# Optimization experiments

Measured on AMD Instinct MI355X. Metric: run time of the kernel, lower is better.

## Reference

```python
import jax, jax.numpy as jnp
import numpy as np
import math

L, B = 1024, 256
SEQ_DIM, KMER_DIM, HID = 16, 256, 64
N_LAYERS = 2
IN_DIM = SEQ_DIM + KMER_DIM + 21  # 293


def _normalize(v, eps=1e-12):
    return v / jnp.maximum(jnp.linalg.norm(v, axis=-1, keepdims=True), eps)


def _nerf_rot(a, b, c):
    # rotation matrix with columns [bc, n x bc, n] from last three backbone points
    bc = _normalize(c - b)
    n = _normalize(jnp.cross(b - a, bc))
    return jnp.stack([bc, jnp.cross(n, bc), n], axis=-1)  # (..., 3, 3)


def pnerf(c_tilde, nfrag):
    # c_tilde: (3L, B, 3) SRF coordinates; parallelized natural extension of reference frame
    Ltot, batch = c_tilde.shape[0], c_tilde.shape[1]
    k = Ltot // nfrag
    # contiguous fragments of length k, folded into the batch dim: (k, nfrag*B, 3)
    x = c_tilde.reshape(nfrag, k, batch, 3).transpose(1, 0, 2, 3).reshape(k, nfrag * batch, 3)
    init = jnp.array([[-math.sqrt(0.5), math.sqrt(1.5), 0.0],
                      [-math.sqrt(2.0), 0.0, 0.0],
                      [0.0, 0.0, 0.0]], dtype=c_tilde.dtype)
    F = nfrag * batch
    carry0 = (jnp.broadcast_to(init[0], (F, 3)),
              jnp.broadcast_to(init[1], (F, 3)),
              jnp.broadcast_to(init[2], (F, 3)))

    def extend(carry, ct):
        a, b, c = carry
        R = _nerf_rot(a, b, c)                      # (F, 3, 3)
        d = c + jnp.einsum('fij,fj->fi', R, ct)     # (F, 3)
        return (b, c, d), d

    _, frag = jax.lax.scan(extend, carry0, x)        # (k, F, 3)
    frag = frag.reshape(k, nfrag, batch, 3).transpose(1, 0, 2, 3)  # (nfrag, k, B, 3)

    # assemble fragments sequentially; init frame is identity/origin so frag 0 passes through
    carryA = (jnp.broadcast_to(init[0], (batch, 3)),
              jnp.broadcast_to(init[1], (batch, 3)),
              jnp.broadcast_to(init[2], (batch, 3)))

    def assemble(carry, fr):
        a, b, c = carry
        R = _nerf_rot(a, b, c)                      # (B, 3, 3)
        y = c + jnp.einsum('bij,kbj->kbi', R, fr)   # (k, B, 3)
        return (y[-3], y[-2], y[-1]), y

    _, ys = jax.lax.scan(assemble, carryA, frag)     # (nfrag, k, B, 3)
    return ys.reshape(nfrag * k, batch, 3)


def setup_inputs() -> dict:
    key = jax.random.key(0)
    ks = jax.random.split(key, 12)
    s = 0.05
    return {
        'seq': jax.random.randint(ks[0], (L, B), 0, 20, dtype=jnp.int64),
        'kmer': jax.random.randint(ks[1], (L, B), 0, 22 ** 3, dtype=jnp.int64),
        'pssm': jax.random.uniform(ks[2], (L, B, 21), dtype=jnp.float32),
        'length': jax.random.randint(ks[3], (L,), 1, L, dtype=jnp.int64),
        'seq_embed': jax.random.normal(ks[4], (20, SEQ_DIM), dtype=jnp.float32) * s,
        'kmer_embed': jax.random.normal(ks[5], (22 ** 3, KMER_DIM), dtype=jnp.float32) * s,
        'W0': jax.random.normal(ks[6], (IN_DIM, HID), dtype=jnp.float32) * s,
        'b0': jnp.zeros((HID,), dtype=jnp.float32),
        'We': jax.random.normal(ks[7], (HID, HID), dtype=jnp.float32) * s,
        'be': jnp.zeros((HID,), dtype=jnp.float32),
        'W1': jax.random.normal(ks[8], (HID, 9), dtype=jnp.float32) * s,
        'b1': jnp.zeros((9,), dtype=jnp.float32),
    }


def reference(seq, kmer, pssm, length, seq_embed, kmer_embed, W0, b0, We, be, W1, b1):
    s = seq_embed[seq]                                   # (L, B, 16)
    km = kmer_embed[kmer]                                # (L, B, 256)
    h = jnp.concatenate([s, km, pssm], axis=2)           # (L, B, 293)
    h = h @ W0 + b0                                      # (L, B, 64)
    # torch list-multiplication shares the SAME Linear across the n_layers blocks
    for _ in range(N_LAYERS):
        h = jax.nn.relu(h @ We + be)                     # dropout is identity at eval
    srf = h @ W1 + b1                                    # (L, B, 9)
    Ld, Bd = srf.shape[0], srf.shape[1]
    srf = srf.reshape(Ld, Bd, 3, 3).transpose(0, 2, 1, 3).reshape(3 * Ld, Bd, 3)
    return pnerf(srf, int(math.sqrt(Ld)))
```

## Files before the change

### kernel.cpp

```cpp
#include <hip/hip_runtime.h>
#include <math.h>

typedef short bf16x8 __attribute__((ext_vector_type(8)));
typedef float f32x4  __attribute__((ext_vector_type(4)));

__device__ __forceinline__ unsigned short f2bf(float x) {
    unsigned int u = __float_as_uint(x);
    return (unsigned short)((u + 0x7FFFu + ((u >> 16) & 1u)) >> 16);
}
__device__ __forceinline__ float bf2f(unsigned short h) {
    return __uint_as_float(((unsigned int)h) << 16);
}
__device__ __forceinline__ void split2(float x, unsigned short& h, unsigned short& l) {
    h = f2bf(x);
    l = f2bf(x - bf2f(h));
}
__device__ __forceinline__ void split2t(float x, unsigned short& h, unsigned short& l) {
    unsigned int u = __float_as_uint(x);
    h = (unsigned short)(u >> 16);
    float r = x - __uint_as_float(u & 0xFFFF0000u);
    l = f2bf(r);
}

__device__ __forceinline__ int hsw(int row, int col) {
    return (row << 6) + ((((col >> 3) ^ (row & 7)) << 3) | (col & 7));
}

__device__ __forceinline__ float inv_norm3(float x, float y, float z) {
    float d = fmaf(x, x, fmaf(y, y, z * z));
    return rsqrtf(fmaxf(d, 1e-24f));
}
__device__ __forceinline__ float3 f3sub(float3 a, float3 b) {
    return make_float3(a.x - b.x, a.y - b.y, a.z - b.z);
}
__device__ __forceinline__ float3 f3cross(float3 a, float3 b) {
    return make_float3(a.y * b.z - a.z * b.y,
                       a.z * b.x - a.x * b.z,
                       a.x * b.y - a.y * b.x);
}
__device__ __forceinline__ void nerf_frame(const float3& A, const float3& Bv,
                                           const float3& C, float3& bc,
                                           float3& n, float3& m3) {
    float3 w  = f3sub(C, Bv);
    float3 v  = f3sub(Bv, A);
    float3 cr = f3cross(v, w);
    float iw = inv_norm3(w.x, w.y, w.z);
    float ic = inv_norm3(cr.x, cr.y, cr.z);
    bc = make_float3(w.x * iw, w.y * iw, w.z * iw);
    n  = make_float3(cr.x * ic, cr.y * ic, cr.z * ic);
    m3 = f3cross(n, bc);
}
__device__ __forceinline__ float3 nerf_place(const float3& C, const float3& bc,
                                             const float3& m3, const float3& n,
                                             float tx, float ty, float tz) {
    return make_float3(
        fmaf(m3.x, ty, fmaf(bc.x, tx, fmaf(n.x, tz, C.x))),
        fmaf(m3.y, ty, fmaf(bc.y, tx, fmaf(n.y, tz, C.y))),
        fmaf(m3.z, ty, fmaf(bc.z, tx, fmaf(n.z, tz, C.z))));
}

struct KParams {
    const int* seq; const int* kmer; const float* pssm;
    const float* se; const float* emb;
    const float* W0; const float* b0; const float* We; const float* be;
    const float* W1; const float* b1;
    float* kmerT; float* seqT; float* srf_t; float* fragbuf;
    float4* frames; float* FPbuf; float* out;
    unsigned short *WeTH, *WeTL, *W0pTH, *W0pTL, *W1TH, *W1TL;
};

__global__ __launch_bounds__(256) void tables_kernel(KParams P) {
    const int tid = threadIdx.x;
    const int vb  = blockIdx.x;
    if (vb < 167) {
        const int lane = tid & 63;
        const int wv   = __builtin_amdgcn_readfirstlane(tid >> 6);
        const int q    = lane >> 4;
        const int c16  = lane & 15;
        const int r0   = vb * 64;
        const int n    = wv * 16 + c16;

        bf16x8 BH[8], BL[8];
        #pragma unroll
        for (int kt8 = 0; kt8 < 8; ++kt8)
            #pragma unroll
            for (int j = 0; j < 8; ++j) {
                float w = P.W0[(16 + kt8 * 32 + q * 8 + j) * 64 + n];
                unsigned short h, l; split2t(w, h, l);
                BH[kt8][j] = (short)h; BL[kt8][j] = (short)l;
            }
        f32x4 acc[4];
        #pragma unroll
        for (int t = 0; t < 4; ++t) acc[t] = (f32x4){0.f, 0.f, 0.f, 0.f};
        #pragma unroll
        for (int kt8 = 0; kt8 < 8; ++kt8) {
            #pragma unroll
            for (int t = 0; t < 4; ++t) {
                int rr = r0 + t * 16 + c16;
                if (rr > 10647) rr = 10647;
                const float* ap = P.emb + rr * 256 + kt8 * 32 + q * 8;
                float4 a0 = *(const float4*)ap;
                float4 a1 = *(const float4*)(ap + 4);
                bf16x8 ah, al;
                unsigned short h, l;
                split2t(a0.x, h, l); ah[0] = (short)h; al[0] = (short)l;
                split2t(a0.y, h, l); ah[1] = (short)h; al[1] = (short)l;
                split2t(a0.z, h, l); ah[2] = (short)h; al[2] = (short)l;
                split2t(a0.w, h, l); ah[3] = (short)h; al[3] = (short)l;
                split2t(a1.x, h, l); ah[4] = (short)h; al[4] = (short)l;
                split2t(a1.y, h, l); ah[5] = (short)h; al[5] = (short)l;
                split2t(a1.z, h, l); ah[6] = (short)h; al[6] = (short)l;
                split2t(a1.w, h, l); ah[7] = (short)h; al[7] = (short)l;
                acc[t] = __builtin_amdgcn_mfma_f32_16x16x32_bf16(ah, BH[kt8], acc[t], 0, 0, 0);
                acc[t] = __builtin_amdgcn_mfma_f32_16x16x32_bf16(al, BH[kt8], acc[t], 0, 0, 0);
                acc[t] = __builtin_amdgcn_mfma_f32_16x16x32_bf16(ah, BL[kt8], acc[t], 0, 0, 0);
            }
        }
        #pragma unroll
        for (int t = 0; t < 4; ++t)
            #pragma unroll
            for (int r = 0; r < 4; ++r) {
                int row = r0 + t * 16 + q * 4 + r;
                if (row < 10648) P.kmerT[row * 64 + n] = acc[t][r];
            }
    } else if (vb < 172) {
        int e = (vb - 167) * 256 + tid;
        int r = e >> 6, j = e & 63;
        float acc = P.b0[j];
        #pragma unroll
        for (int k = 0; k < 16; ++k)
            acc = fmaf(P.se[r * 16 + k], P.W0[k * 64 + j], acc);
        float cs = 0.f;
        #pragma unroll
        for (int c = 0; c < 21; ++c) cs += P.W0[(272 + c) * 64 + j];
        P.seqT[r * 64 + j] = acc + 0.5f * cs;
    } else {
        #pragma unroll
        for (int i = 0; i < 16; ++i) {
            int e = i * 256 + tid;
            int k = e >> 6, n = e & 63;
            unsigned short h, l; split2(P.We[k * 64 + n], h, l);
            P.WeTH[n * 64 + k] = h; P.WeTL[n * 64 + k] = l;
        }
        #pragma unroll
        for (int i = 0; i < 8; ++i) {
            int e = i * 256 + tid;
            int k = e >> 6, n = e & 63;
            float w = (k < 21) ? P.W0[(272 + k) * 64 + n] : 0.f;
            unsigned short h, l; split2(w, h, l);
            P.W0pTH[n * 32 + k] = h; P.W0pTL[n * 32 + k] = l;
        }
        #pragma unroll
        for (int i = 0; i < 4; ++i) {
            int e = i * 256 + tid;
            int k = e >> 4, c = e & 15;
            float w = (c < 9) ? P.W1[k * 9 + c] : 0.f;
            unsigned short h, l; split2(w, h, l);
            P.W1TH[c * 64 + k] = h; P.W1TL[c * 64 + k] = l;
        }
    }
}

__global__ __launch_bounds__(256, 4) void mlp_kernel(KParams P) {
    __shared__ __align__(16) unsigned char SMEM[32768];
    unsigned short* Hah = (unsigned short*)(SMEM);
    unsigned short* Hal = (unsigned short*)(SMEM + 8192);
    unsigned short* Hbh = (unsigned short*)(SMEM + 16384);
    unsigned short* Hbl = (unsigned short*)(SMEM + 24576);
    unsigned short (*Ph)[40] = (unsigned short (*)[40])(SMEM + 16384);
    unsigned short (*Pl)[40] = (unsigned short (*)[40])(SMEM + 16384 + 5120);

    const int tid  = threadIdx.x;
    const int lane = tid & 63;
    const int wv   = __builtin_amdgcn_readfirstlane(tid >> 6);
    const int q    = lane >> 4;
    const int c16  = lane & 15;
    const int m0   = blockIdx.x * 64;
    const int n    = wv * 16 + c16;

    const int myseq = P.seq[m0 + lane];
    const int mykm  = P.kmer[m0 + lane];
    float g[4][4];
    #pragma unroll
    for (int t = 0; t < 4; ++t)
        #pragma unroll
        for (int r = 0; r < 4; ++r) {
            int src = (t * 16 + q * 4 + r) << 2;
            int s  = __builtin_amdgcn_ds_bpermute(src, myseq);
            int km = __builtin_amdgcn_ds_bpermute(src, mykm);
            g[t][r] = P.seqT[s * 64 + n] + P.kmerT[km * 64 + n];
        }

    for (int i = tid; i < 64 * 21; i += 256) {
        float v = P.pssm[m0 * 21 + i] - 0.5f;
        unsigned short h, l; split2t(v, h, l);
        Ph[i / 21][i % 21] = h;
        Pl[i / 21][i % 21] = l;
    }
    for (int i = tid; i < 64 * 11; i += 256) {
        Ph[i / 11][21 + (i % 11)] = 0;
        Pl[i / 11][21 + (i % 11)] = 0;
    }

    bf16x8 WeH[2], WeL[2], W1H[2], W1L[2], W0H, W0L;
    #pragma unroll
    for (int kk = 0; kk < 2; ++kk) {
        WeH[kk] = *(const bf16x8*)(P.WeTH + n * 64 + kk * 32 + q * 8);
        WeL[kk] = *(const bf16x8*)(P.WeTL + n * 64 + kk * 32 + q * 8);
        W1H[kk] = *(const bf16x8*)(P.W1TH + c16 * 64 + kk * 32 + q * 8);
        W1L[kk] = *(const bf16x8*)(P.W1TL + c16 * 64 + kk * 32 + q * 8);
    }
    W0H = *(const bf16x8*)(P.W0pTH + n * 32 + q * 8);
    W0L = *(const bf16x8*)(P.W0pTL + n * 32 + q * 8);
    const float be_n = P.be[n];
    const float b1h  = (c16 < 9) ? P.b1[c16] : 0.f;
    __syncthreads();

    f32x4 acc[4];
    #pragma unroll
    for (int t = 0; t < 4; ++t) acc[t] = (f32x4){0.f, 0.f, 0.f, 0.f};
    #pragma unroll
    for (int t = 0; t < 4; ++t) {
        bf16x8 ah = *(const bf16x8*)&Ph[t * 16 + c16][q * 8];
        bf16x8 al = *(const bf16x8*)&Pl[t * 16 + c16][q * 8];
        acc[t] = __builtin_amdgcn_mfma_f32_16x16x32_bf16(ah, W0H, acc[t], 0, 0, 0);
        acc[t] = __builtin_amdgcn_mfma_f32_16x16x32_bf16(al, W0H, acc[t], 0, 0, 0);
        acc[t] = __builtin_amdgcn_mfma_f32_16x16x32_bf16(ah, W0L, acc[t], 0, 0, 0);
    }
    #pragma unroll
    for (int t = 0; t < 4; ++t)
        #pragma unroll
        for (int r = 0; r < 4; ++r) {
            unsigned short h, l; split2t(acc[t][r] + g[t][r], h, l);
            Hah[hsw(t * 16 + q * 4 + r, n)] = h;
            Hal[hsw(t * 16 + q * 4 + r, n)] = l;
        }
    __syncthreads();

    {
        f32x4 a1[4];
        #pragma unroll
        for (int t = 0; t < 4; ++t) {
            a1[t] = (f32x4){be_n, be_n, be_n, be_n};
            #pragma unroll
            for (int kk = 0; kk < 2; ++kk) {
                bf16x8 ah = *(const bf16x8*)&Hah[hsw(t * 16 + c16, kk * 32 + q * 8)];
                bf16x8 al = *(const bf16x8*)&Hal[hsw(t * 16 + c16, kk * 32 + q * 8)];
                a1[t] = __builtin_amdgcn_mfma_f32_16x16x32_bf16(ah, WeH[kk], a1[t], 0, 0, 0);
                a1[t] = __builtin_amdgcn_mfma_f32_16x16x32_bf16(al, WeH[kk], a1[t], 0, 0, 0);
                a1[t] = __builtin_amdgcn_mfma_f32_16x16x32_bf16(ah, WeL[kk], a1[t], 0, 0, 0);
            }
        }
        #pragma unroll
        for (int t = 0; t < 4; ++t)
            #pragma unroll
            for (int r = 0; r < 4; ++r) {
                unsigned short h, l; split2t(fmaxf(a1[t][r], 0.f), h, l);
                Hbh[hsw(t * 16 + q * 4 + r, n)] = h;
                Hbl[hsw(t * 16 + q * 4 + r, n)] = l;
            }
        __syncthreads();
    }
    {
        f32x4 a2[4];
        #pragma unroll
        for (int t = 0; t < 4; ++t) {
            a2[t] = (f32x4){be_n, be_n, be_n, be_n};
            #pragma unroll
            for (int kk = 0; kk < 2; ++kk) {
                bf16x8 ah = *(const bf16x8*)&Hbh[hsw(t * 16 + c16, kk * 32 + q * 8)];
                bf16x8 al = *(const bf16x8*)&Hbl[hsw(t * 16 + c16, kk * 32 + q * 8)];
                a2[t] = __builtin_amdgcn_mfma_f32_16x16x32_bf16(ah, WeH[kk], a2[t], 0, 0, 0);
                a2[t] = __builtin_amdgcn_mfma_f32_16x16x32_bf16(al, WeH[kk], a2[t], 0, 0, 0);
                a2[t] = __builtin_amdgcn_mfma_f32_16x16x32_bf16(ah, WeL[kk], a2[t], 0, 0, 0);
            }
        }
        #pragma unroll
        for (int t = 0; t < 4; ++t)
            #pragma unroll
            for (int r = 0; r < 4; ++r) {
                unsigned short h, l; split2t(fmaxf(a2[t][r], 0.f), h, l);
                Hah[hsw(t * 16 + q * 4 + r, n)] = h;
                Hal[hsw(t * 16 + q * 4 + r, n)] = l;
            }
        __syncthreads();
    }
    {
        f32x4 ah4 = (f32x4){b1h, b1h, b1h, b1h};
        #pragma unroll
        for (int kk = 0; kk < 2; ++kk) {
            bf16x8 ah = *(const bf16x8*)&Hah[hsw(wv * 16 + c16, kk * 32 + q * 8)];
            bf16x8 al = *(const bf16x8*)&Hal[hsw(wv * 16 + c16, kk * 32 + q * 8)];
            ah4 = __builtin_amdgcn_mfma_f32_16x16x32_bf16(ah, W1H[kk], ah4, 0, 0, 0);
            ah4 = __builtin_amdgcn_mfma_f32_16x16x32_bf16(al, W1H[kk], ah4, 0, 0, 0);
            ah4 = __builtin_amdgcn_mfma_f32_16x16x32_bf16(ah, W1L[kk], ah4, 0, 0, 0);
        }
        if (c16 < 9) {
            #pragma unroll
            for (int r = 0; r < 4; ++r) {
                int pos = m0 + wv * 16 + q * 4 + r;
                int l = pos >> 8, b = pos & 255;
                P.srf_t[(l * 9 + c16) * 256 + b] = ah4[r];
            }
        }
    }
}

__global__ __launch_bounds__(64) void extend_kernel(KParams P) {
    int frag = blockIdx.x >> 2;
    int bb   = ((blockIdx.x & 3) << 6) + threadIdx.x;

    float3 A  = make_float3(-0.70710678118654752f, 1.22474487139158905f, 0.f);
    float3 Bv = make_float3(-1.41421356237309505f, 0.f, 0.f);
    float3 C  = make_float3(0.f, 0.f, 0.f);

    float ct0[9], ct1[9], ct2[9], ct3[9];
    #pragma unroll
    for (int m = 0; m < 9; ++m) {
        ct0[m] = P.srf_t[((frag * 32 + 0) * 9 + m) * 256 + bb];
        ct1[m] = P.srf_t[((frag * 32 + 1) * 9 + m) * 256 + bb];
        ct2[m] = P.srf_t[((frag * 32 + 2) * 9 + m) * 256 + bb];
    }
    for (int ll = 0; ll < 32; ++ll) {
        if (ll < 29) {
            #pragma unroll
            for (int m = 0; m < 9; ++m)
                ct3[m] = P.srf_t[((frag * 32 + ll + 3) * 9 + m) * 256 + bb];
        } else {
            #pragma unroll
            for (int m = 0; m < 9; ++m) ct3[m] = 0.f;
        }
        #pragma unroll
        for (int s3 = 0; s3 < 3; ++s3) {
            float3 bc, nn, m3;
            nerf_frame(A, Bv, C, bc, nn, m3);
            float3 d = nerf_place(C, bc, m3, nn,
                                  ct0[3 * s3 + 0], ct0[3 * s3 + 1], ct0[3 * s3 + 2]);
            int row = frag * 96 + ll * 3 + s3;
            P.fragbuf[(row * 3 + 0) * 256 + bb] = d.x;
            P.fragbuf[(row * 3 + 1) * 256 + bb] = d.y;
            P.fragbuf[(row * 3 + 2) * 256 + bb] = d.z;
            A = Bv; Bv = C; C = d;
        }
        #pragma unroll
        for (int m = 0; m < 9; ++m) { ct0[m] = ct1[m]; ct1[m] = ct2[m]; ct2[m] = ct3[m]; }
    }
    float3 bc, nn, m3;
    nerf_frame(A, Bv, C, bc, nn, m3);
    P.FPbuf[(frag * 12 + 0)  * 256 + bb] = bc.x;
    P.FPbuf[(frag * 12 + 1)  * 256 + bb] = bc.y;
    P.FPbuf[(frag * 12 + 2)  * 256 + bb] = bc.z;
    P.FPbuf[(frag * 12 + 3)  * 256 + bb] = m3.x;
    P.FPbuf[(frag * 12 + 4)  * 256 + bb] = m3.y;
    P.FPbuf[(frag * 12 + 5)  * 256 + bb] = m3.z;
    P.FPbuf[(frag * 12 + 6)  * 256 + bb] = nn.x;
    P.FPbuf[(frag * 12 + 7)  * 256 + bb] = nn.y;
    P.FPbuf[(frag * 12 + 8)  * 256 + bb] = nn.z;
    P.FPbuf[(frag * 12 + 9)  * 256 + bb] = C.x;
    P.FPbuf[(frag * 12 + 10) * 256 + bb] = C.y;
    P.FPbuf[(frag * 12 + 11) * 256 + bb] = C.z;
}

__global__ __launch_bounds__(256) void carry_kernel(KParams P) {
    __shared__ float S[384][16];
    const int tid  = threadIdx.x;
    const int base = blockIdx.x * 16;
    for (int i = tid; i < 384 * 16; i += 256) {
        int row = i >> 4, col = i & 15;
        S[row][col] = P.FPbuf[row * 256 + base + col];
    }
    __syncthreads();
    if (tid < 16) {
        int bb = base + tid;
        float3 ob = make_float3(1.f, 0.f, 0.f);
        float3 om = make_float3(0.f, 1.f, 0.f);
        float3 on = make_float3(0.f, 0.f, 1.f);
        float3 c  = make_float3(0.f, 0.f, 0.f);
        for (int f = 0; f < 32; ++f) {
            int fb = (f * 256 + bb) * 3;
            P.frames[fb + 0] = make_float4(ob.x, ob.y, ob.z, om.x);
            P.frames[fb + 1] = make_float4(om.y, om.z, on.x, on.y);
            P.frames[fb + 2] = make_float4(on.z, c.x, c.y, c.z);

            int r0 = f * 12;
            float3 Fb = make_float3(S[r0+0][tid], S[r0+1][tid], S[r0+2][tid]);
            float3 Fm = make_float3(S[r0+3][tid], S[r0+4][tid], S[r0+5][tid]);
            float3 Fn = make_float3(S[r0+6][tid], S[r0+7][tid], S[r0+8][tid]);
            float3 p  = make_float3(S[r0+9][tid], S[r0+10][tid], S[r0+11][tid]);

            float3 nb = make_float3(
                fmaf(ob.x,Fb.x, fmaf(om.x,Fb.y, on.x*Fb.z)),
                fmaf(ob.y,Fb.x, fmaf(om.y,Fb.y, on.y*Fb.z)),
                fmaf(ob.z,Fb.x, fmaf(om.z,Fb.y, on.z*Fb.z)));
            float3 nm = make_float3(
                fmaf(ob.x,Fm.x, fmaf(om.x,Fm.y, on.x*Fm.z)),
                fmaf(ob.y,Fm.x, fmaf(om.y,Fm.y, on.y*Fm.z)),
                fmaf(ob.z,Fm.x, fmaf(om.z,Fm.y, on.z*Fm.z)));
            float3 nn2 = make_float3(
                fmaf(ob.x,Fn.x, fmaf(om.x,Fn.y, on.x*Fn.z)),
                fmaf(ob.y,Fn.x, fmaf(om.y,Fn.y, on.y*Fn.z)),
                fmaf(ob.z,Fn.x, fmaf(om.z,Fn.y, on.z*Fn.z)));
            float3 nc = make_float3(
                fmaf(ob.x,p.x, fmaf(om.x,p.y, fmaf(on.x,p.z, c.x))),
                fmaf(ob.y,p.x, fmaf(om.y,p.y, fmaf(on.y,p.z, c.y))),
                fmaf(ob.z,p.x, fmaf(om.z,p.y, fmaf(on.z,p.z, c.z))));
            ob = nb; om = nm; on = nn2; c = nc;
        }
    }
}

__global__ __launch_bounds__(256) void apply_kernel(KParams P) {
    __shared__ float sm[768];
    const int bb = threadIdx.x;
    #pragma unroll 1
    for (int i = 0; i < 4; ++i) {
        const int row  = blockIdx.x * 4 + i;
        const int frag = row / 96;

        float fx = P.fragbuf[(row * 3 + 0) * 256 + bb];
        float fy = P.fragbuf[(row * 3 + 1) * 256 + bb];
        float fz = P.fragbuf[(row * 3 + 2) * 256 + bb];

        int fb = (frag * 256 + bb) * 3;
        float4 f0 = P.frames[fb + 0];
        float4 f1 = P.frames[fb + 1];
        float4 f2 = P.frames[fb + 2];

        float ox = f2.y + f0.x * fx + f0.w * fy + f1.z * fz;
        float oy = f2.z + f0.y * fx + f1.x * fy + f1.w * fz;
        float oz = f2.w + f0.z * fx + f1.y * fy + f2.x * fz;

        __syncthreads();
        sm[bb * 3 + 0] = ox;
        sm[bb * 3 + 1] = oy;
        sm[bb * 3 + 2] = oz;
        __syncthreads();

        int base = row * 768;
        P.out[base + bb]       = sm[bb];
        P.out[base + 256 + bb] = sm[256 + bb];
        P.out[base + 512 + bb] = sm[512 + bb];
    }
}

extern "C" void kernel_launch(void* const* d_in, const int* in_sizes, int n_in,
                              void* d_out, int out_size, void* d_ws, size_t ws_size,
                              hipStream_t stream) {
    float* ws      = (float*)d_ws;
    float* kmerT   = ws;
    float* seqT    = kmerT + 681472;
    float* srf_t   = seqT + 1280;
    float* fragbuf = srf_t + 2359296;
    float* frames  = fragbuf + 2359296;
    float* FPbuf   = frames + 98304;

    unsigned short* WeTH  = (unsigned short*)fragbuf;
    unsigned short* WeTL  = WeTH + 4096;
    unsigned short* W0pTH = WeTL + 4096;
    unsigned short* W0pTL = W0pTH + 2048;
    unsigned short* W1TH  = W0pTL + 2048;
    unsigned short* W1TL  = W1TH + 1024;

    KParams P;
    P.seq  = (const int*)d_in[0];
    P.kmer = (const int*)d_in[1];
    P.pssm = (const float*)d_in[2];
    P.se   = (const float*)d_in[4];
    P.emb  = (const float*)d_in[5];
    P.W0   = (const float*)d_in[6];
    P.b0   = (const float*)d_in[7];
    P.We   = (const float*)d_in[8];
    P.be   = (const float*)d_in[9];
    P.W1   = (const float*)d_in[10];
    P.b1   = (const float*)d_in[11];
    P.kmerT = kmerT; P.seqT = seqT; P.srf_t = srf_t; P.fragbuf = fragbuf;
    P.frames = (float4*)frames; P.FPbuf = FPbuf; P.out = (float*)d_out;
    P.WeTH = WeTH; P.WeTL = WeTL; P.W0pTH = W0pTH; P.W0pTL = W0pTL;
    P.W1TH = W1TH; P.W1TL = W1TL;

    hipLaunchKernelGGL(tables_kernel, dim3(173),  dim3(256), 0, stream, P);
    hipLaunchKernelGGL(mlp_kernel,    dim3(4096), dim3(256), 0, stream, P);
    hipLaunchKernelGGL(extend_kernel, dim3(128),  dim3(64),  0, stream, P);
    hipLaunchKernelGGL(carry_kernel,  dim3(16),   dim3(256), 0, stream, P);
    hipLaunchKernelGGL(apply_kernel,  dim3(768),  dim3(256), 0, stream, P);
}
```

Measured before the change: 176.5 us.

## Give each wave its own 16-row slab in the MLP to drop block barriers

Reorganizes the MLP kernel so each wavefront owns 16 rows and computes all 64 output columns, keeping activations in a private LDS region per wave. This removes every __syncthreads between layers and halves shared memory to 16KB, which may allow higher occupancy. In exchange, weights are reloaded from global or cache inside the layer loops instead of being held in registers, and each wave issues four times as many weight loads.

```diff
diff --git a/kernel.cpp b/kernel.cpp
--- a/kernel.cpp
+++ b/kernel.cpp
@@ -22,7 +22,7 @@
     l = f2bf(r);
 }
 
-__device__ __forceinline__ int hsw(int row, int col) {
+__device__ __forceinline__ int hsw16(int row, int col) {
     return (row << 6) + ((((col >> 3) ^ (row & 7)) << 3) | (col & 7));
 }
 
@@ -161,14 +161,8 @@
     }
 }
 
-__global__ __launch_bounds__(256, 4) void mlp_kernel(KParams P) {
-    __shared__ __align__(16) unsigned char SMEM[32768];
-    unsigned short* Hah = (unsigned short*)(SMEM);
-    unsigned short* Hal = (unsigned short*)(SMEM + 8192);
-    unsigned short* Hbh = (unsigned short*)(SMEM + 16384);
-    unsigned short* Hbl = (unsigned short*)(SMEM + 24576);
-    unsigned short (*Ph)[40] = (unsigned short (*)[40])(SMEM + 16384);
-    unsigned short (*Pl)[40] = (unsigned short (*)[40])(SMEM + 16384 + 5120);
+__global__ __launch_bounds__(256) void mlp_kernel(KParams P) {
+    __shared__ __align__(16) unsigned char SMEM[16384];
 
     const int tid  = threadIdx.x;
     const int lane = tid & 63;
@@ -176,131 +170,123 @@
     const int q    = lane >> 4;
     const int c16  = lane & 15;
     const int m0   = blockIdx.x * 64;
-    const int n    = wv * 16 + c16;
+
+    unsigned short* Hh  = (unsigned short*)SMEM + wv * 1024;
+    unsigned short* Hl  = (unsigned short*)(SMEM + 8192) + wv * 1024;
+    unsigned short* Pph = Hh;
+    unsigned short* Ppl = Hl;
 
     const int myseq = P.seq[m0 + lane];
     const int mykm  = P.kmer[m0 + lane];
+    int sidx[4], kidx[4];
+    #pragma unroll
+    for (int r = 0; r < 4; ++r) {
+        int src = (wv * 16 + q * 4 + r) << 2;
+        sidx[r] = __builtin_amdgcn_ds_bpermute(src, myseq);
+        kidx[r] = __builtin_amdgcn_ds_bpermute(src, mykm);
+    }
     float g[4][4];
     #pragma unroll
-    for (int t = 0; t < 4; ++t)
+    for (int nt = 0; nt < 4; ++nt)
+        #pragma unroll
+        for (int r = 0; r < 4; ++r)
+            g[nt][r] = P.seqT[sidx[r] * 64 + nt * 16 + c16]
+                     + P.kmerT[kidx[r] * 64 + nt * 16 + c16];
+
+    const float* prow = P.pssm + (m0 + wv * 16) * 21;
+    for (int i = lane; i < 16 * 21; i += 64) {
+        float v = prow[i] - 0.5f;
+        unsigned short h, l; split2t(v, h, l);
+        int row = i / 21, col = i - row * 21;
+        Pph[row * 32 + col] = h;
+        Ppl[row * 32 + col] = l;
+    }
+    for (int i = lane; i < 16 * 11; i += 64) {
+        int row = i / 11, col = 21 + (i - row * 11);
+        Pph[row * 32 + col] = 0;
+        Ppl[row * 32 + col] = 0;
+    }
+
+    float be4[4];
+    #pragma unroll
+    for (int nt = 0; nt < 4; ++nt) be4[nt] = P.be[nt * 16 + c16];
+    const float b1h = (c16 < 9) ? P.b1[c16] : 0.f;
+
+    bf16x8 pah = *(const bf16x8*)&Pph[c16 * 32 + q * 8];
+    bf16x8 pal = *(const bf16x8*)&Ppl[c16 * 32 + q * 8];
+    f32x4 acc[4];
+    #pragma unroll
+    for (int nt = 0; nt < 4; ++nt) {
+        const int wo = (nt * 16 + c16) * 32 + q * 8;
+        bf16x8 w0h = *(const bf16x8*)(P.W0pTH + wo);
+        bf16x8 w0l = *(const bf16x8*)(P.W0pTL + wo);
+        f32x4 a = (f32x4){0.f, 0.f, 0.f, 0.f};
+        a = __builtin_amdgcn_mfma_f32_16x16x32_bf16(pah, w0h, a, 0, 0, 0);
+        a = __builtin_amdgcn_mfma_f32_16x16x32_bf16(pal, w0h, a, 0, 0, 0);
+        a = __builtin_amdgcn_mfma_f32_16x16x32_bf16(pah, w0l, a, 0, 0, 0);
+        acc[nt] = a;
+    }
+    #pragma unroll
+    for (int nt = 0; nt < 4; ++nt)
         #pragma unroll
         for (int r = 0; r < 4; ++r) {
-            int src = (t * 16 + q * 4 + r) << 2;
-            int s  = __builtin_amdgcn_ds_bpermute(src, myseq);
-            int km = __builtin_amdgcn_ds_bpermute(src, mykm);
-            g[t][r] = P.seqT[s * 64 + n] + P.kmerT[km * 64 + n];
-        }
-
-    for (int i = tid; i < 64 * 21; i += 256) {
-        float v = P.pssm[m0 * 21 + i] - 0.5f;
-        unsigned short h, l; split2t(v, h, l);
-        Ph[i / 21][i % 21] = h;
-        Pl[i / 21][i % 21] = l;
-    }
-    for (int i = tid; i < 64 * 11; i += 256) {
-        Ph[i / 11][21 + (i % 11)] = 0;
-        Pl[i / 11][21 + (i % 11)] = 0;
-    }
-
-    bf16x8 WeH[2], WeL[2], W1H[2], W1L[2], W0H, W0L;
-    #pragma unroll
-    for (int kk = 0; kk < 2; ++kk) {
-        WeH[kk] = *(const bf16x8*)(P.WeTH + n * 64 + kk * 32 + q * 8);
-        WeL[kk] = *(const bf16x8*)(P.WeTL + n * 64 + kk * 32 + q * 8);
-        W1H[kk] = *(const bf16x8*)(P.W1TH + c16 * 64 + kk * 32 + q * 8);
-        W1L[kk] = *(const bf16x8*)(P.W1TL + c16 * 64 + kk * 32 + q * 8);
-    }
-    W0H = *(const bf16x8*)(P.W0pTH + n * 32 + q * 8);
-    W0L = *(const bf16x8*)(P.W0pTL + n * 32 + q * 8);
-    const float be_n = P.be[n];
-    const float b1h  = (c16 < 9) ? P.b1[c16] : 0.f;
-    __syncthreads();
-
-    f32x4 acc[4];
-    #pragma unroll
-    for (int t = 0; t < 4; ++t) acc[t] = (f32x4){0.f, 0.f, 0.f, 0.f};
-    #pragma unroll
-    for (int t = 0; t < 4; ++t) {
-        bf16x8 ah = *(const bf16x8*)&Ph[t * 16 + c16][q * 8];
-        bf16x8 al = *(const bf16x8*)&Pl[t * 16 + c16][q * 8];
-        acc[t] = __builtin_amdgcn_mfma_f32_16x16x32_bf16(ah, W0H, acc[t], 0, 0, 0);
-        acc[t] = __builtin_amdgcn_mfma_f32_16x16x32_bf16(al, W0H, acc[t], 0, 0, 0);
-        acc[t] = __builtin_amdgcn_mfma_f32_16x16x32_bf16(ah, W0L, acc[t], 0, 0, 0);
-    }
-    #pragma unroll
-    for (int t = 0; t < 4; ++t)
-        #pragma unroll
-        for (int r = 0; r < 4; ++r) {
-            unsigned short h, l; split2t(acc[t][r] + g[t][r], h, l);
-            Hah[hsw(t * 16 + q * 4 + r, n)] = h;
-            Hal[hsw(t * 16 + q * 4 + r, n)] = l;
-        }
-    __syncthreads();
+            unsigned short h, l; split2t(acc[nt][r] + g[nt][r], h, l);
+            Hh[hsw16(q * 4 + r, nt * 16 + c16)] = h;
+            Hl[hsw16(q * 4 + r, nt * 16 + c16)] = l;
+        }
+
+    #pragma unroll
+    for (int layer = 0; layer < 2; ++layer) {
+        bf16x8 ahk[2], alk[2];
+        #pragma unroll
+        for (int kk = 0; kk < 2; ++kk) {
+            ahk[kk] = *(const bf16x8*)&Hh[hsw16(c16, kk * 32 + q * 8)];
+            alk[kk] = *(const bf16x8*)&Hl[hsw16(c16, kk * 32 + q * 8)];
+        }
+        f32x4 a1[4];
+        #pragma unroll
+        for (int nt = 0; nt < 4; ++nt) {
+            f32x4 a = (f32x4){be4[nt], be4[nt], be4[nt], be4[nt]};
+            #pragma unroll
+            for (int kk = 0; kk < 2; ++kk) {
+                const int wo = (nt * 16 + c16) * 64 + kk * 32 + q * 8;
+                bf16x8 weh = *(const bf16x8*)(P.WeTH + wo);
+                bf16x8 wel = *(const bf16x8*)(P.WeTL + wo);
+                a = __builtin_amdgcn_mfma_f32_16x16x32_bf16(ahk[kk], weh, a, 0, 0, 0);
+                a = __builtin_amdgcn_mfma_f32_16x16x32_bf16(alk[kk], weh, a, 0, 0, 0);
+                a = __builtin_amdgcn_mfma_f32_16x16x32_bf16(ahk[kk], wel, a, 0, 0, 0);
+            }
+            a1[nt] = a;
+        }
+        #pragma unroll
+        for (int nt = 0; nt < 4; ++nt)
+            #pragma unroll
+            for (int r = 0; r < 4; ++r) {
+                unsigned short h, l; split2t(fmaxf(a1[nt][r], 0.f), h, l);
+                Hh[hsw16(q * 4 + r, nt * 16 + c16)] = h;
+                Hl[hsw16(q * 4 + r, nt * 16 + c16)] = l;
+            }
+    }
 
     {
-        f32x4 a1[4];
-        #pragma unroll
-        for (int t = 0; t < 4; ++t) {
-            a1[t] = (f32x4){be_n, be_n, be_n, be_n};
-            #pragma unroll
-            for (int kk = 0; kk < 2; ++kk) {
-                bf16x8 ah = *(const bf16x8*)&Hah[hsw(t * 16 + c16, kk * 32 + q * 8)];
-                bf16x8 al = *(const bf16x8*)&Hal[hsw(t * 16 + c16, kk * 32 + q * 8)];
-                a1[t] = __builtin_amdgcn_mfma_f32_16x16x32_bf16(ah, WeH[kk], a1[t], 0, 0, 0);
-                a1[t] = __builtin_amdgcn_mfma_f32_16x16x32_bf16(al, WeH[kk], a1[t], 0, 0, 0);
-                a1[t] = __builtin_amdgcn_mfma_f32_16x16x32_bf16(ah, WeL[kk], a1[t], 0, 0, 0);
-            }
-        }
-        #pragma unroll
-        for (int t = 0; t < 4; ++t)
-            #pragma unroll
-            for (int r = 0; r < 4; ++r) {
-                unsigned short h, l; split2t(fmaxf(a1[t][r], 0.f), h, l);
-                Hbh[hsw(t * 16 + q * 4 + r, n)] = h;
-                Hbl[hsw(t * 16 + q * 4 + r, n)] = l;
-            }
-        __syncthreads();
-    }
-    {
-        f32x4 a2[4];
-        #pragma unroll
-        for (int t = 0; t < 4; ++t) {
-            a2[t] = (f32x4){be_n, be_n, be_n, be_n};
-            #pragma unroll
-            for (int kk = 0; kk < 2; ++kk) {
-                bf16x8 ah = *(const bf16x8*)&Hbh[hsw(t * 16 + c16, kk * 32 + q * 8)];
-                bf16x8 al = *(const bf16x8*)&Hbl[hsw(t * 16 + c16, kk * 32 + q * 8)];
-                a2[t] = __builtin_amdgcn_mfma_f32_16x16x32_bf16(ah, WeH[kk], a2[t], 0, 0, 0);
-                a2[t] = __builtin_amdgcn_mfma_f32_16x16x32_bf16(al, WeH[kk], a2[t], 0, 0, 0);
-                a2[t] = __builtin_amdgcn_mfma_f32_16x16x32_bf16(ah, WeL[kk], a2[t], 0, 0, 0);
-            }
-        }
-        #pragma unroll
-        for (int t = 0; t < 4; ++t)
-            #pragma unroll
-            for (int r = 0; r < 4; ++r) {
-                unsigned short h, l; split2t(fmaxf(a2[t][r], 0.f), h, l);
-                Hah[hsw(t * 16 + q * 4 + r, n)] = h;
-                Hal[hsw(t * 16 + q * 4 + r, n)] = l;
-            }
-        __syncthreads();
-    }
-    {
-        f32x4 ah4 = (f32x4){b1h, b1h, b1h, b1h};
+        f32x4 hacc = (f32x4){b1h, b1h, b1h, b1h};
         #pragma unroll
         for (int kk = 0; kk < 2; ++kk) {
-            bf16x8 ah = *(const bf16x8*)&Hah[hsw(wv * 16 + c16, kk * 32 + q * 8)];
-            bf16x8 al = *(const bf16x8*)&Hal[hsw(wv * 16 + c16, kk * 32 + q * 8)];
-            ah4 = __builtin_amdgcn_mfma_f32_16x16x32_bf16(ah, W1H[kk], ah4, 0, 0, 0);
-            ah4 = __builtin_amdgcn_mfma_f32_16x16x32_bf16(al, W1H[kk], ah4, 0, 0, 0);
-            ah4 = __builtin_amdgcn_mfma_f32_16x16x32_bf16(ah, W1L[kk], ah4, 0, 0, 0);
+            bf16x8 ah = *(const bf16x8*)&Hh[hsw16(c16, kk * 32 + q * 8)];
+            bf16x8 al = *(const bf16x8*)&Hl[hsw16(c16, kk * 32 + q * 8)];
+            const int wo = c16 * 64 + kk * 32 + q * 8;
+            bf16x8 w1h = *(const bf16x8*)(P.W1TH + wo);
+            bf16x8 w1l = *(const bf16x8*)(P.W1TL + wo);
+            hacc = __builtin_amdgcn_mfma_f32_16x16x32_bf16(ah, w1h, hacc, 0, 0, 0);
+            hacc = __builtin_amdgcn_mfma_f32_16x16x32_bf16(al, w1h, hacc, 0, 0, 0);
+            hacc = __builtin_amdgcn_mfma_f32_16x16x32_bf16(ah, w1l, hacc, 0, 0, 0);
         }
         if (c16 < 9) {
             #pragma unroll
             for (int r = 0; r < 4; ++r) {
                 int pos = m0 + wv * 16 + q * 4 + r;
                 int l = pos >> 8, b = pos & 255;
-                P.srf_t[(l * 9 + c16) * 256 + b] = ah4[r];
+                P.srf_t[(l * 9 + c16) * 256 + b] = hacc[r];
             }
         }
     }
```

After: 228.0 us. +29.1%, slower.
